# Kernel tuning notes

Measured on AMD Instinct MI355X. Metric: run time of the kernel, lower is better.

## Reference

```python
import jax, jax.numpy as jnp
import numpy as np
import math

B, SQ, SK, DQ, DK, DV = 8, 1024, 1024, 512, 512, 512


def setup_inputs() -> dict:
    key = jax.random.key(0)
    ks = jax.random.split(key, 12)
    s = lambda fan_in: 1.0 / math.sqrt(fan_in)
    return {
        "Q": jax.random.normal(ks[0], (B, SQ, DQ), jnp.float32),
        "K": jax.random.normal(ks[1], (B, SK, DK), jnp.float32),
        "Wq": jax.random.uniform(ks[2], (DV, DQ), jnp.float32, -s(DQ), s(DQ)),
        "bq": jax.random.uniform(ks[3], (DV,), jnp.float32, -s(DQ), s(DQ)),
        "Wk": jax.random.uniform(ks[4], (DV, DK), jnp.float32, -s(DK), s(DK)),
        "bk": jax.random.uniform(ks[5], (DV,), jnp.float32, -s(DK), s(DK)),
        "Wv": jax.random.uniform(ks[6], (DV, DK), jnp.float32, -s(DK), s(DK)),
        "bv": jax.random.uniform(ks[7], (DV,), jnp.float32, -s(DK), s(DK)),
        "Wo": jax.random.uniform(ks[8], (DV, DV), jnp.float32, -s(DV), s(DV)),
        "bo": jax.random.uniform(ks[9], (DV,), jnp.float32, -s(DV), s(DV)),
        "num_heads": 8,
    }


def reference(Q, K, Wq, bq, Wk, bk, Wv, bv, Wo, bo, num_heads):
    dim_V = Wq.shape[0]
    dh = dim_V // num_heads
    b, sq, _ = Q.shape
    sk = K.shape[1]
    # projections (torch Linear: x @ W.T + b)
    Qp = Q @ Wq.T + bq                      # [B, Sq, Dv]
    Kp = K @ Wk.T + bk                      # [B, Sk, Dv]
    Vp = K @ Wv.T + bv                      # [B, Sk, Dv]
    # manual head split (split along feature, cat along batch) == reshape to heads
    Qh = Qp.reshape(b, sq, num_heads, dh)   # [B, Sq, H, dh]
    Kh = Kp.reshape(b, sk, num_heads, dh)
    Vh = Vp.reshape(b, sk, num_heads, dh)
    # NOTE: scale is sqrt(dim_V), not sqrt(head_dim), as in the source.
    scores = jnp.einsum("bqhd,bkhd->bhqk", Qh, Kh) / jnp.sqrt(
        jnp.asarray(dim_V, Qh.dtype))
    A = jax.nn.softmax(scores, axis=-1)     # [B, H, Sq, Sk]
    ctx = jnp.einsum("bhqk,bkhd->bqhd", A, Vh)
    O = (Qh + ctx).reshape(b, sq, dim_V)    # residual on projected Q, merge heads
    O = O + jax.nn.relu(O @ Wo.T + bo)      # FFN residual
    return O
```

## Files before the change

### kernel.cpp

```cpp
#include <hip/hip_runtime.h>

typedef unsigned short u16;
typedef __attribute__((ext_vector_type(8))) short short8;
typedef __attribute__((ext_vector_type(4))) float f32x4;
typedef __attribute__((ext_vector_type(2))) unsigned uint2v;

__device__ __forceinline__ u16 f2bf(float f) {
  union { float f; unsigned u; } v; v.f = f;
  unsigned r = v.u + 0x7FFFu + ((v.u >> 16) & 1u);
  return (u16)(r >> 16);
}
__device__ __forceinline__ float bf2f(u16 u) {
  union { unsigned u; float f; } v; v.u = ((unsigned)u) << 16;
  return v.f;
}
__device__ __forceinline__ void gload_lds16(const u16* g, u16* l) {
  __builtin_amdgcn_global_load_lds((const __attribute__((address_space(1))) void*)g,
                                   (__attribute__((address_space(3))) void*)l,
                                   16, 0, 0);
}

#if __has_builtin(__builtin_amdgcn_exp2f)
#define EXP2(x) __builtin_amdgcn_exp2f(x)
#else
#define EXP2(x) exp2f(x)
#endif

#define BATCH 8
#define SEQ   1024
#define DIM   512
#define NH    8
#define DH    64
#define MROWS (BATCH * SEQ)

__global__ void cvt_w(const float* __restrict__ Wq, const float* __restrict__ Wk,
                      const float* __restrict__ Wv, const float* __restrict__ Wo,
                      u16* __restrict__ out) {
  const float* s = (blockIdx.y == 0) ? Wq : (blockIdx.y == 1) ? Wk
                   : (blockIdx.y == 2) ? Wv : Wo;
  const float4* src = (const float4*)s;
  u16* dst = out + (size_t)blockIdx.y * (DIM * DIM);
  int i = blockIdx.x * 256 + threadIdx.x;
  float4 v = src[i];
  ushort4 r;
  r.x = f2bf(v.x); r.y = f2bf(v.y); r.z = f2bf(v.z); r.w = f2bf(v.w);
  *(ushort4*)&dst[i * 4] = r;
}

__device__ __forceinline__ void gemm_core(const u16* __restrict__ A,
                                          const u16* __restrict__ W,
                                          u16* ldsA, u16* ldsB,
                                          int tid, int m0, int n0,
                                          f32x4 acc[4][4]) {
  const int lane = tid & 63;
  const int wv = tid >> 6;
  const int wr = wv >> 1, wc = wv & 1;
  const int lr = lane & 15, lg = lane >> 4;
  const int wbase = tid & 192;

#define STAGE(buf, kt)                                                          \
  {                                                                             \
    _Pragma("unroll")                                                           \
    for (int i = 0; i < 2; ++i) {                                               \
      const int T = i * 256 + tid;                                              \
      const int row = T & 127, kc = T >> 7;                                     \
      const int koff = (kt) * 32 + kc * 8;                                      \
      gload_lds16(A + (size_t)(m0 + row) * DIM + koff,                          \
                  ldsA + (buf) * 4096 + (i * 256 + wbase) * 8);                 \
      gload_lds16(W + (size_t)(n0 + row) * DIM + koff,                          \
                  ldsB + (buf) * 4096 + (i * 256 + wbase) * 8);                 \
    }                                                                           \
  }

  STAGE(0, 0);
  __syncthreads();
  int cur = 0;
#pragma unroll 1
  for (int kt = 0; kt < 16; ++kt) {
    if (kt < 15) STAGE(cur ^ 1, kt + 1);
    short8 av[4], bw[4];
#pragma unroll
    for (int m = 0; m < 4; ++m)
      av[m] = *(const short8*)(ldsA + cur * 4096 + (lg * 128 + wr * 64 + m * 16 + lr) * 8);
#pragma unroll
    for (int n = 0; n < 4; ++n)
      bw[n] = *(const short8*)(ldsB + cur * 4096 + (lg * 128 + wc * 64 + n * 16 + lr) * 8);
#pragma unroll
    for (int m = 0; m < 4; ++m)
#pragma unroll
      for (int n = 0; n < 4; ++n)
        acc[m][n] = __builtin_amdgcn_mfma_f32_16x16x32_bf16(av[m], bw[n], acc[m][n], 0, 0, 0);
    __syncthreads();
    cur ^= 1;
  }
#undef STAGE
}

__global__ __launch_bounds__(256, 2) void proj_gemm(
    const float* __restrict__ Qf, const float* __restrict__ Kf,
    const u16* __restrict__ Wbf,
    const float* __restrict__ bq, const float* __restrict__ bk,
    const float* __restrict__ bv,
    u16* __restrict__ Qp, u16* __restrict__ Kp, u16* __restrict__ VpT) {
  __shared__ alignas(16) u16 ldsA[2 * 4096];
  __shared__ alignas(16) u16 ldsB[2 * 4096];

  const int tid = threadIdx.x;
  const int z = blockIdx.z;
  const int m0 = blockIdx.x * 128;
  const int n0 = blockIdx.y * 128;

  const float* A32 = (z == 0) ? Qf : Kf;
  const u16* W = Wbf + (size_t)z * (DIM * DIM);
  const float* bias = (z == 0) ? bq : (z == 1) ? bk : bv;

  const int lane = tid & 63;
  const int wv = tid >> 6;
  const int wr = wv >> 1, wc = wv & 1;
  const int lr = lane & 15, lg = lane >> 4;
  const int wbase = tid & 192;

  float4 fA[2][2];

#define PISSUE_A(kt)                                                            \
  {                                                                             \
    _Pragma("unroll")                                                           \
    for (int i = 0; i < 2; ++i) {                                               \
      const int T = i * 256 + tid;                                              \
      const int row = T >> 2, cc = T & 3;                                       \
      const float* g = A32 + (size_t)(m0 + row) * DIM + (kt) * 32 + cc * 8;     \
      fA[i][0] = *(const float4*)g;                                             \
      fA[i][1] = *(const float4*)(g + 4);                                       \
    }                                                                           \
  }

#define PSTAGE_B(buf, kt)                                                       \
  {                                                                             \
    _Pragma("unroll")                                                           \
    for (int i = 0; i < 2; ++i) {                                               \
      const int T = i * 256 + tid;                                              \
      const int row = T & 127, kc = T >> 7;                                     \
      gload_lds16(W + (size_t)(n0 + row) * DIM + (kt) * 32 + kc * 8,            \
                  ldsB + (buf) * 4096 + (i * 256 + wbase) * 8);                 \
    }                                                                           \
  }

#define PWRITE_A(buf)                                                           \
  {                                                                             \
    _Pragma("unroll")                                                           \
    for (int i = 0; i < 2; ++i) {                                               \
      const int T = i * 256 + tid;                                              \
      const int row = T >> 2, cc = T & 3;                                       \
      unsigned w0, w1, w2, w3;                                                  \
      asm("v_cvt_pk_bf16_f32 %0, %1, %2" : "=v"(w0) : "v"(fA[i][0].x), "v"(fA[i][0].y)); \
      asm("v_cvt_pk_bf16_f32 %0, %1, %2" : "=v"(w1) : "v"(fA[i][0].z), "v"(fA[i][0].w)); \
      asm("v_cvt_pk_bf16_f32 %0, %1, %2" : "=v"(w2) : "v"(fA[i][1].x), "v"(fA[i][1].y)); \
      asm("v_cvt_pk_bf16_f32 %0, %1, %2" : "=v"(w3) : "v"(fA[i][1].z), "v"(fA[i][1].w)); \
      union { unsigned u[4]; short8 s; } pk_;                                   \
      pk_.u[0] = w0; pk_.u[1] = w1; pk_.u[2] = w2; pk_.u[3] = w3;               \
      *(short8*)(ldsA + (buf) * 4096 + cc * 1024 + row * 8) = pk_.s;            \
    }                                                                           \
  }

  f32x4 acc[4][4] = {};

  PISSUE_A(0);
  PSTAGE_B(0, 0);
  PWRITE_A(0);
  __syncthreads();

  int cur = 0;
#pragma unroll 1
  for (int kt = 0; kt < 16; ++kt) {
    if (kt < 15) { PISSUE_A(kt + 1); PSTAGE_B(cur ^ 1, kt + 1); }
    short8 av[4], bw[4];
#pragma unroll
    for (int m = 0; m < 4; ++m)
      av[m] = *(const short8*)(ldsA + cur * 4096 + (lg * 128 + wr * 64 + m * 16 + lr) * 8);
#pragma unroll
    for (int n = 0; n < 4; ++n)
      bw[n] = *(const short8*)(ldsB + cur * 4096 + (lg * 128 + wc * 64 + n * 16 + lr) * 8);
#pragma unroll
    for (int m = 0; m < 4; ++m)
#pragma unroll
      for (int n = 0; n < 4; ++n)
        acc[m][n] = __builtin_amdgcn_mfma_f32_16x16x32_bf16(av[m], bw[n], acc[m][n], 0, 0, 0);
    if (kt < 15) PWRITE_A(cur ^ 1);
    __syncthreads();
    cur ^= 1;
  }
#undef PISSUE_A
#undef PSTAGE_B
#undef PWRITE_A

  float bn[4];
#pragma unroll
  for (int n = 0; n < 4; ++n) bn[n] = bias[n0 + wc * 64 + n * 16 + lr];

  if (z < 2) {
    u16* outp = (z == 0) ? Qp : Kp;
#pragma unroll
    for (int m = 0; m < 4; ++m)
#pragma unroll
      for (int n = 0; n < 4; ++n)
#pragma unroll
        for (int r = 0; r < 4; ++r) {
          const int row = m0 + wr * 64 + m * 16 + lg * 4 + r;
          const int col = n0 + wc * 64 + n * 16 + lr;
          outp[(size_t)row * DIM + col] = f2bf(acc[m][n][r] + bn[n]);
        }
  } else {
#pragma unroll
    for (int m = 0; m < 4; ++m)
#pragma unroll
      for (int n = 0; n < 4; ++n) {
        const int grow = m0 + wr * 64 + m * 16 + lg * 4;
        const int b = grow >> 10;
        const int s = grow & 1023;
        const int col = n0 + wc * 64 + n * 16 + lr;
        ushort4 pk;
        pk.x = f2bf(acc[m][n][0] + bn[n]);
        pk.y = f2bf(acc[m][n][1] + bn[n]);
        pk.z = f2bf(acc[m][n][2] + bn[n]);
        pk.w = f2bf(acc[m][n][3] + bn[n]);
        *(ushort4*)&VpT[(size_t)b * (DIM * SEQ) + (size_t)col * SEQ + s] = pk;
      }
  }
}

__global__ __launch_bounds__(512, 4) void attn_kernel(
    const u16* __restrict__ Qp, const u16* __restrict__ Kp,
    const u16* __restrict__ VpT, u16* __restrict__ Opre) {
  __shared__ alignas(16) u16 klds[2][4096];
  __shared__ alignas(16) u16 vlds[2][4096];
  __shared__ alignas(16) u16 plds[8][64 * 16];

  const int tid = threadIdx.x;
  const int lane = tid & 63, wv = tid >> 6;
  const int lr = lane & 15, lg = lane >> 4;
  const int q0 = blockIdx.y * 128;
  const int b = blockIdx.x >> 3, h = blockIdx.x & 7;
  const size_t rowbase = (size_t)b * SEQ;
  const int hoff = h * DH;

  const float csc = 0.063762f;
  short8 aq[2];
#pragma unroll
  for (int t = 0; t < 2; ++t) {
    short8 raw = *(const short8*)(Qp + (rowbase + q0 + wv * 16 + lr) * DIM +
                                  hoff + t * 32 + lg * 8);
    short8 s;
#pragma unroll
    for (int j = 0; j < 8; ++j) s[j] = (short)f2bf(bf2f((u16)raw[j]) * csc);
    aq[t] = s;
  }

  short8 ones;
#pragma unroll
  for (int j = 0; j < 8; ++j) ones[j] = (short)0x3F80;

#define STAGEKV(buf, kt)                                                        \
  {                                                                             \
    const int ks0_ = (kt) * 64;                                                 \
    const int rr = tid & 63, cc = tid >> 6;                                     \
    gload_lds16(Kp + (rowbase + ks0_ + rr) * DIM + hoff + cc * 8,               \
                &klds[buf][tid * 8]);                                           \
    gload_lds16(VpT + (size_t)b * (DIM * SEQ) + (size_t)(hoff + rr) * SEQ +     \
                    ks0_ + cc * 8,                                              \
                &vlds[buf][tid * 8]);                                           \
  }

  u16* pw = &plds[wv][0];
  unsigned pbase = (unsigned)(uintptr_t)(__attribute__((address_space(3))) u16*)pw;
  const unsigned ta00 = pbase + (unsigned)lg * 128u;
  const unsigned ta01 = ta00 + 128u;
  const unsigned ta10 = ta00 + 1024u;
  const unsigned ta11 = ta00 + 1152u;

  f32x4 l_acc = {};
  f32x4 o_acc[4] = {};

  STAGEKV(0, 0);
  __syncthreads();

  int cur = 0;
#pragma unroll 1
  for (int kt = 0; kt < 16; ++kt) {
    if (kt < 15) STAGEKV(cur ^ 1, kt + 1);

    f32x4 sa[4] = {};
    __builtin_amdgcn_s_setprio(1);
#pragma unroll
    for (int t = 0; t < 2; ++t)
#pragma unroll
      for (int f = 0; f < 4; ++f) {
        short8 bk_ = *(const short8*)(&klds[cur][((lg + 4 * t) * 64 + f * 16 + lr) * 8]);
        sa[f] = __builtin_amdgcn_mfma_f32_16x16x32_bf16(aq[t], bk_, sa[f], 0, 0, 0);
      }
    __builtin_amdgcn_s_setprio(0);

    short8 bvf[8];
#pragma unroll
    for (int n = 0; n < 4; ++n)
#pragma unroll
      for (int t = 0; t < 2; ++t)
        bvf[n * 2 + t] = *(const short8*)(&vlds[cur][((lg + 4 * t) * 64 + n * 16 + lr) * 8]);

#pragma unroll
    for (int f = 0; f < 4; ++f) {
      float p0 = EXP2(sa[f][0]);
      float p1 = EXP2(sa[f][1]);
      float p2 = EXP2(sa[f][2]);
      float p3 = EXP2(sa[f][3]);
      unsigned lo, hi;
      asm("v_cvt_pk_bf16_f32 %0, %1, %2" : "=v"(lo) : "v"(p0), "v"(p1));
      asm("v_cvt_pk_bf16_f32 %0, %1, %2" : "=v"(hi) : "v"(p2), "v"(p3));
      uint2v pk; pk.x = lo; pk.y = hi;
      *(uint2v*)&pw[(f * 16 + lr) * 16 + lg * 4] = pk;
    }

    asm volatile("s_waitcnt lgkmcnt(0)" ::: "memory");
    uint2v t00, t01, t10, t11;
    asm volatile("ds_read_b64_tr_b16 %0, %1" : "=v"(t00) : "v"(ta00));
    asm volatile("ds_read_b64_tr_b16 %0, %1" : "=v"(t01) : "v"(ta01));
    asm volatile("ds_read_b64_tr_b16 %0, %1" : "=v"(t10) : "v"(ta10));
    asm volatile("ds_read_b64_tr_b16 %0, %1" : "=v"(t11) : "v"(ta11));
    asm volatile("s_waitcnt lgkmcnt(0)" ::: "memory");
    __builtin_amdgcn_sched_barrier(0);

    short8 ap[2];
    {
      union { unsigned u[4]; short8 s; } u0, u1;
      u0.u[0] = t00.x; u0.u[1] = t00.y; u0.u[2] = t01.x; u0.u[3] = t01.y;
      u1.u[0] = t10.x; u1.u[1] = t10.y; u1.u[2] = t11.x; u1.u[3] = t11.y;
      ap[0] = u0.s; ap[1] = u1.s;
    }

    __builtin_amdgcn_s_setprio(1);
#pragma unroll
    for (int n = 0; n < 4; ++n)
#pragma unroll
      for (int t = 0; t < 2; ++t)
        o_acc[n] = __builtin_amdgcn_mfma_f32_16x16x32_bf16(ap[t], bvf[n * 2 + t], o_acc[n], 0, 0, 0);
    l_acc = __builtin_amdgcn_mfma_f32_16x16x32_bf16(ap[0], ones, l_acc, 0, 0, 0);
    l_acc = __builtin_amdgcn_mfma_f32_16x16x32_bf16(ap[1], ones, l_acc, 0, 0, 0);
    __builtin_amdgcn_s_setprio(0);

    __syncthreads();
    cur ^= 1;
  }
#undef STAGEKV

  float inv[4];
#pragma unroll
  for (int r = 0; r < 4; ++r) inv[r] = 1.0f / l_acc[r];
#pragma unroll
  for (int n = 0; n < 4; ++n)
#pragma unroll
    for (int r = 0; r < 4; ++r) {
      const size_t row = rowbase + q0 + wv * 16 + lg * 4 + r;
      const int col = hoff + n * 16 + lr;
      const float ctx = o_acc[n][r] * inv[r];
      const float qv = bf2f(Qp[row * DIM + col]);
      Opre[row * DIM + col] = f2bf(qv + ctx);
    }
}

__global__ __launch_bounds__(256, 2) void ffn_gemm(
    const u16* __restrict__ Opre, const u16* __restrict__ Wo_bf,
    const float* __restrict__ bo, float* __restrict__ out) {
  __shared__ alignas(16) u16 ldsA[2 * 4096];
  __shared__ alignas(16) u16 ldsB[2 * 4096];

  const int tid = threadIdx.x;
  const int m0 = blockIdx.x * 128;
  const int n0 = blockIdx.y * 128;

  f32x4 acc[4][4] = {};
  gemm_core(Opre, Wo_bf, ldsA, ldsB, tid, m0, n0, acc);

  const int lane = tid & 63;
  const int wv = tid >> 6;
  const int wr = wv >> 1, wc = wv & 1;
  const int lr = lane & 15, lg = lane >> 4;

  float bn[4];
#pragma unroll
  for (int n = 0; n < 4; ++n) bn[n] = bo[n0 + wc * 64 + n * 16 + lr];

#pragma unroll
  for (int m = 0; m < 4; ++m)
#pragma unroll
    for (int n = 0; n < 4; ++n)
#pragma unroll
      for (int r = 0; r < 4; ++r) {
        const int row = m0 + wr * 64 + m * 16 + lg * 4 + r;
        const int col = n0 + wc * 64 + n * 16 + lr;
        const float v = acc[m][n][r] + bn[n];
        const float o = bf2f(Opre[(size_t)row * DIM + col]);
        out[(size_t)row * DIM + col] = o + fmaxf(v, 0.f);
      }
}

extern "C" void kernel_launch(void* const* d_in, const int* in_sizes, int n_in,
                              void* d_out, int out_size, void* d_ws, size_t ws_size,
                              hipStream_t stream) {
  const float* Q  = (const float*)d_in[0];
  const float* K  = (const float*)d_in[1];
  const float* Wq = (const float*)d_in[2];
  const float* bq = (const float*)d_in[3];
  const float* Wk = (const float*)d_in[4];
  const float* bk = (const float*)d_in[5];
  const float* Wv = (const float*)d_in[6];
  const float* bv = (const float*)d_in[7];
  const float* Wo = (const float*)d_in[8];
  const float* bo = (const float*)d_in[9];

  char* ws = (char*)d_ws;
  const size_t SZ = (size_t)MROWS * DIM * sizeof(u16);
  const size_t WSZ = 4 * (size_t)(DIM * DIM) * sizeof(u16);
  u16* Wbf  = (u16*)(ws + 0);
  u16* Qp   = (u16*)(ws + WSZ);
  u16* Kp   = (u16*)((char*)Qp + SZ);
  u16* VpT  = (u16*)((char*)Kp + SZ);
  u16* Opre = (u16*)((char*)VpT + SZ);

  cvt_w<<<dim3(256, 4), 256, 0, stream>>>(Wq, Wk, Wv, Wo, Wbf);
  proj_gemm<<<dim3(64, 4, 3), 256, 0, stream>>>(Q, K, Wbf, bq, bk, bv, Qp, Kp, VpT);
  attn_kernel<<<dim3(64, 8), 512, 0, stream>>>(Qp, Kp, VpT, Opre);
  ffn_gemm<<<dim3(64, 4), 256, 0, stream>>>(Opre, Wbf + 3 * (DIM * DIM), bo, (float*)d_out);
}
```

Before: 83.17 us.

## Deepen fp32 A prefetch to two stages and pad LDS A rows in proj_gemm

```diff
diff --git a/kernel.cpp b/kernel.cpp
--- a/kernel.cpp
+++ b/kernel.cpp
@@ -32,6 +32,9 @@
 #define NH    8
 #define DH    64
 #define MROWS (BATCH * SEQ)
+
+#define ASTRIDE 1040
+#define ABUF    (4 * ASTRIDE)
 
 __global__ void cvt_w(const float* __restrict__ Wq, const float* __restrict__ Wk,
                       const float* __restrict__ Wv, const float* __restrict__ Wo,
@@ -96,13 +99,13 @@
 #undef STAGE
 }
 
-__global__ __launch_bounds__(256, 2) void proj_gemm(
+__global__ __launch_bounds__(256, 3) void proj_gemm(
     const float* __restrict__ Qf, const float* __restrict__ Kf,
     const u16* __restrict__ Wbf,
     const float* __restrict__ bq, const float* __restrict__ bk,
     const float* __restrict__ bv,
     u16* __restrict__ Qp, u16* __restrict__ Kp, u16* __restrict__ VpT) {
-  __shared__ alignas(16) u16 ldsA[2 * 4096];
+  __shared__ alignas(16) u16 ldsA[2 * ABUF];
   __shared__ alignas(16) u16 ldsB[2 * 4096];
 
   const int tid = threadIdx.x;
@@ -120,17 +123,17 @@
   const int lr = lane & 15, lg = lane >> 4;
   const int wbase = tid & 192;
 
-  float4 fA[2][2];
-
-#define PISSUE_A(kt)                                                            \
+  float4 fA0[2][2], fA1[2][2];
+
+#define PISSUE_A(kt, R)                                                         \
   {                                                                             \
     _Pragma("unroll")                                                           \
     for (int i = 0; i < 2; ++i) {                                               \
       const int T = i * 256 + tid;                                              \
       const int row = T >> 2, cc = T & 3;                                       \
       const float* g = A32 + (size_t)(m0 + row) * DIM + (kt) * 32 + cc * 8;     \
-      fA[i][0] = *(const float4*)g;                                             \
-      fA[i][1] = *(const float4*)(g + 4);                                       \
+      R[i][0] = *(const float4*)g;                                              \
+      R[i][1] = *(const float4*)(g + 4);                                        \
     }                                                                           \
   }
 
@@ -145,38 +148,44 @@
     }                                                                           \
   }
 
-#define PWRITE_A(buf)                                                           \
+#define PWRITE_A(buf, R)                                                        \
   {                                                                             \
     _Pragma("unroll")                                                           \
     for (int i = 0; i < 2; ++i) {                                               \
       const int T = i * 256 + tid;                                              \
       const int row = T >> 2, cc = T & 3;                                       \
       unsigned w0, w1, w2, w3;                                                  \
-      asm("v_cvt_pk_bf16_f32 %0, %1, %2" : "=v"(w0) : "v"(fA[i][0].x), "v"(fA[i][0].y)); \
-      asm("v_cvt_pk_bf16_f32 %0, %1, %2" : "=v"(w1) : "v"(fA[i][0].z), "v"(fA[i][0].w)); \
-      asm("v_cvt_pk_bf16_f32 %0, %1, %2" : "=v"(w2) : "v"(fA[i][1].x), "v"(fA[i][1].y)); \
-      asm("v_cvt_pk_bf16_f32 %0, %1, %2" : "=v"(w3) : "v"(fA[i][1].z), "v"(fA[i][1].w)); \
+      asm("v_cvt_pk_bf16_f32 %0, %1, %2" : "=v"(w0) : "v"(R[i][0].x), "v"(R[i][0].y)); \
+      asm("v_cvt_pk_bf16_f32 %0, %1, %2" : "=v"(w1) : "v"(R[i][0].z), "v"(R[i][0].w)); \
+      asm("v_cvt_pk_bf16_f32 %0, %1, %2" : "=v"(w2) : "v"(R[i][1].x), "v"(R[i][1].y)); \
+      asm("v_cvt_pk_bf16_f32 %0, %1, %2" : "=v"(w3) : "v"(R[i][1].z), "v"(R[i][1].w)); \
       union { unsigned u[4]; short8 s; } pk_;                                   \
       pk_.u[0] = w0; pk_.u[1] = w1; pk_.u[2] = w2; pk_.u[3] = w3;               \
-      *(short8*)(ldsA + (buf) * 4096 + cc * 1024 + row * 8) = pk_.s;            \
+      *(short8*)(ldsA + (buf) * ABUF + cc * ASTRIDE + row * 8) = pk_.s;         \
     }                                                                           \
   }
 
   f32x4 acc[4][4] = {};
 
-  PISSUE_A(0);
+  PISSUE_A(0, fA0);
   PSTAGE_B(0, 0);
-  PWRITE_A(0);
+  PWRITE_A(0, fA0);
+  PISSUE_A(1, fA1);
   __syncthreads();
 
   int cur = 0;
 #pragma unroll 1
   for (int kt = 0; kt < 16; ++kt) {
-    if (kt < 15) { PISSUE_A(kt + 1); PSTAGE_B(cur ^ 1, kt + 1); }
+    if (kt < 14) {
+      if ((kt & 1) == 0) PISSUE_A(kt + 2, fA0)
+      else               PISSUE_A(kt + 2, fA1)
+    }
+    if (kt < 15) PSTAGE_B(cur ^ 1, kt + 1);
     short8 av[4], bw[4];
 #pragma unroll
     for (int m = 0; m < 4; ++m)
-      av[m] = *(const short8*)(ldsA + cur * 4096 + (lg * 128 + wr * 64 + m * 16 + lr) * 8);
+      av[m] = *(const short8*)(ldsA + cur * ABUF + lg * ASTRIDE +
+                               (wr * 64 + m * 16 + lr) * 8);
 #pragma unroll
     for (int n = 0; n < 4; ++n)
       bw[n] = *(const short8*)(ldsB + cur * 4096 + (lg * 128 + wc * 64 + n * 16 + lr) * 8);
@@ -185,7 +194,10 @@
 #pragma unroll
       for (int n = 0; n < 4; ++n)
         acc[m][n] = __builtin_amdgcn_mfma_f32_16x16x32_bf16(av[m], bw[n], acc[m][n], 0, 0, 0);
-    if (kt < 15) PWRITE_A(cur ^ 1);
+    if (kt < 15) {
+      if ((kt & 1) == 0) PWRITE_A(cur ^ 1, fA1)
+      else               PWRITE_A(cur ^ 1, fA0)
+    }
     __syncthreads();
     cur ^= 1;
   }
```

New measurement: 86.11 us. 1.04x slower.

## Stage fp32 A tiles directly into LDS and convert to bf16 at fragment load

Applied to the files above, without the earlier changes.

```diff
diff --git a/kernel.cpp b/kernel.cpp
--- a/kernel.cpp
+++ b/kernel.cpp
@@ -15,6 +15,11 @@
   return v.f;
 }
 __device__ __forceinline__ void gload_lds16(const u16* g, u16* l) {
+  __builtin_amdgcn_global_load_lds((const __attribute__((address_space(1))) void*)g,
+                                   (__attribute__((address_space(3))) void*)l,
+                                   16, 0, 0);
+}
+__device__ __forceinline__ void gload_lds16f(const float* g, u16* l) {
   __builtin_amdgcn_global_load_lds((const __attribute__((address_space(1))) void*)g,
                                    (__attribute__((address_space(3))) void*)l,
                                    16, 0, 0);
@@ -96,13 +101,13 @@
 #undef STAGE
 }
 
-__global__ __launch_bounds__(256, 2) void proj_gemm(
+__global__ __launch_bounds__(256, 3) void proj_gemm(
     const float* __restrict__ Qf, const float* __restrict__ Kf,
     const u16* __restrict__ Wbf,
     const float* __restrict__ bq, const float* __restrict__ bk,
     const float* __restrict__ bv,
     u16* __restrict__ Qp, u16* __restrict__ Kp, u16* __restrict__ VpT) {
-  __shared__ alignas(16) u16 ldsA[2 * 4096];
+  __shared__ alignas(16) u16 ldsA[2 * 8192];
   __shared__ alignas(16) u16 ldsB[2 * 4096];
 
   const int tid = threadIdx.x;
@@ -120,17 +125,15 @@
   const int lr = lane & 15, lg = lane >> 4;
   const int wbase = tid & 192;
 
-  float4 fA[2][2];
-
-#define PISSUE_A(kt)                                                            \
+  const int schunk = (tid & 7) ^ ((tid >> 3) & 7);
+  const float* abase = A32 + (size_t)(m0 + (tid >> 3)) * DIM + schunk * 4;
+
+#define PSTAGE_A(buf, kt)                                                       \
   {                                                                             \
     _Pragma("unroll")                                                           \
-    for (int i = 0; i < 2; ++i) {                                               \
-      const int T = i * 256 + tid;                                              \
-      const int row = T >> 2, cc = T & 3;                                       \
-      const float* g = A32 + (size_t)(m0 + row) * DIM + (kt) * 32 + cc * 8;     \
-      fA[i][0] = *(const float4*)g;                                             \
-      fA[i][1] = *(const float4*)(g + 4);                                       \
+    for (int i = 0; i < 4; ++i) {                                               \
+      gload_lds16f(abase + (size_t)(i * 32) * DIM + (kt) * 32,                  \
+                   ldsA + (buf) * 8192 + (i * 256 + wbase) * 8);                \
     }                                                                           \
   }
 
@@ -145,38 +148,35 @@
     }                                                                           \
   }
 
-#define PWRITE_A(buf)                                                           \
-  {                                                                             \
-    _Pragma("unroll")                                                           \
-    for (int i = 0; i < 2; ++i) {                                               \
-      const int T = i * 256 + tid;                                              \
-      const int row = T >> 2, cc = T & 3;                                       \
-      unsigned w0, w1, w2, w3;                                                  \
-      asm("v_cvt_pk_bf16_f32 %0, %1, %2" : "=v"(w0) : "v"(fA[i][0].x), "v"(fA[i][0].y)); \
-      asm("v_cvt_pk_bf16_f32 %0, %1, %2" : "=v"(w1) : "v"(fA[i][0].z), "v"(fA[i][0].w)); \
-      asm("v_cvt_pk_bf16_f32 %0, %1, %2" : "=v"(w2) : "v"(fA[i][1].x), "v"(fA[i][1].y)); \
-      asm("v_cvt_pk_bf16_f32 %0, %1, %2" : "=v"(w3) : "v"(fA[i][1].z), "v"(fA[i][1].w)); \
-      union { unsigned u[4]; short8 s; } pk_;                                   \
-      pk_.u[0] = w0; pk_.u[1] = w1; pk_.u[2] = w2; pk_.u[3] = w3;               \
-      *(short8*)(ldsA + (buf) * 4096 + cc * 1024 + row * 8) = pk_.s;            \
-    }                                                                           \
-  }
+  const int xr = lr & 7;
+  const int aoff0 = (wr * 64 + lr) * 64 + (((2 * lg) ^ xr) * 8);
+  const int aoff1 = (wr * 64 + lr) * 64 + (((2 * lg + 1) ^ xr) * 8);
 
   f32x4 acc[4][4] = {};
 
-  PISSUE_A(0);
+  PSTAGE_A(0, 0);
   PSTAGE_B(0, 0);
-  PWRITE_A(0);
   __syncthreads();
 
   int cur = 0;
 #pragma unroll 1
   for (int kt = 0; kt < 16; ++kt) {
-    if (kt < 15) { PISSUE_A(kt + 1); PSTAGE_B(cur ^ 1, kt + 1); }
+    if (kt < 15) { PSTAGE_A(cur ^ 1, kt + 1); PSTAGE_B(cur ^ 1, kt + 1); }
+
     short8 av[4], bw[4];
 #pragma unroll
-    for (int m = 0; m < 4; ++m)
-      av[m] = *(const short8*)(ldsA + cur * 4096 + (lg * 128 + wr * 64 + m * 16 + lr) * 8);
+    for (int m = 0; m < 4; ++m) {
+      f32x4 a0 = *(const f32x4*)(ldsA + cur * 8192 + aoff0 + m * 16 * 64);
+      f32x4 a1 = *(const f32x4*)(ldsA + cur * 8192 + aoff1 + m * 16 * 64);
+      unsigned u0, u1, u2, u3;
+      asm("v_cvt_pk_bf16_f32 %0, %1, %2" : "=v"(u0) : "v"(a0[0]), "v"(a0[1]));
+      asm("v_cvt_pk_bf16_f32 %0, %1, %2" : "=v"(u1) : "v"(a0[2]), "v"(a0[3]));
+      asm("v_cvt_pk_bf16_f32 %0, %1, %2" : "=v"(u2) : "v"(a1[0]), "v"(a1[1]));
+      asm("v_cvt_pk_bf16_f32 %0, %1, %2" : "=v"(u3) : "v"(a1[2]), "v"(a1[3]));
+      union { unsigned u[4]; short8 s; } pk_;
+      pk_.u[0] = u0; pk_.u[1] = u1; pk_.u[2] = u2; pk_.u[3] = u3;
+      av[m] = pk_.s;
+    }
 #pragma unroll
     for (int n = 0; n < 4; ++n)
       bw[n] = *(const short8*)(ldsB + cur * 4096 + (lg * 128 + wc * 64 + n * 16 + lr) * 8);
@@ -185,13 +185,11 @@
 #pragma unroll
       for (int n = 0; n < 4; ++n)
         acc[m][n] = __builtin_amdgcn_mfma_f32_16x16x32_bf16(av[m], bw[n], acc[m][n], 0, 0, 0);
-    if (kt < 15) PWRITE_A(cur ^ 1);
     __syncthreads();
     cur ^= 1;
   }
-#undef PISSUE_A
+#undef PSTAGE_A
 #undef PSTAGE_B
-#undef PWRITE_A
 
   float bn[4];
 #pragma unroll
```

Measured after the change: 82.95 us. Within noise of the previous version (-0.3%).
